# Performance work log

Measured on AMD Instinct MI355X. Metric: run time of the kernel, lower is better.

The kernel has to match this reference:

```python
import jax, jax.numpy as jnp
import numpy as np

B, T, C, HS = 8, 2048, 1024, 64

def setup_inputs() -> dict:
    key = jax.random.key(0)
    kx, kq, kk, kv = jax.random.split(key, 4)
    x = jax.random.normal(kx, (B, T, C), dtype=jnp.float32)
    # Linear(C, HS, bias=False) weights, stored as [C, HS] so projection is x @ W
    Wq = jax.random.normal(kq, (C, HS), dtype=jnp.float32) * (C ** -0.5)
    Wk = jax.random.normal(kk, (C, HS), dtype=jnp.float32) * (C ** -0.5)
    Wv = jax.random.normal(kv, (C, HS), dtype=jnp.float32) * (C ** -0.5)
    return {"x": x, "Wq": Wq, "Wk": Wk, "Wv": Wv}

def reference(x, Wq, Wk, Wv):
    Bq, Tq, Cq = x.shape
    q = x @ Wq  # [B,T,HS]
    k = x @ Wk
    v = x @ Wv
    # NOTE: original scales by C**-0.5 with C = embedding_dim (not head_size)
    att = jnp.einsum('bqd,bkd->bqk', q, k) * (Cq ** -0.5)  # [B,T,T]
    causal = jnp.tril(jnp.ones((Tq, Tq), dtype=bool))
    att = jnp.where(causal, att, -jnp.inf)
    att = jax.nn.softmax(att, axis=-1)
    # dropout p=0.0 -> identity
    y = jnp.einsum('bqk,bkd->bqd', att, v)  # [B,T,HS]
    return y
```

## Files before the change

### kernel.cpp

```cpp
#include <hip/hip_runtime.h>
#include <hip/hip_bf16.h>
#include <math.h>

#define B_   8
#define T_   2048
#define C_   1024
#define HS_  64
#define MTOT (B_*T_)

typedef __attribute__((ext_vector_type(8))) short bf16x8;
typedef __attribute__((ext_vector_type(4))) float f32x4;
typedef __attribute__((ext_vector_type(8))) unsigned short u16x8;

static __device__ __forceinline__ unsigned short f2bf(float f) {
    __hip_bfloat16 h = __float2bfloat16(f);
    return *reinterpret_cast<unsigned short*>(&h);
}

__global__ __launch_bounds__(256) void cast_w_kernel(
    const float* __restrict__ Wq, const float* __restrict__ Wk,
    const float* __restrict__ Wv, unsigned short* __restrict__ Wt)
{
    const int tid = threadIdx.x;
    const int col = tid & 63;
    const int kc  = tid >> 6;
    const int mat = blockIdx.y;
    const int k0  = (blockIdx.x * 4 + kc) * 8;
    const float* __restrict__ W = (mat == 0) ? Wq : (mat == 1) ? Wk : Wv;
    const float s = (mat == 0) ? 0.03125f : 1.0f;

    u16x8 o;
#pragma unroll
    for (int i = 0; i < 8; ++i)
        o[i] = f2bf(W[(size_t)(k0 + i) * HS_ + col] * s);
    *(u16x8*)&Wt[(size_t)(mat * 64 + col) * C_ + k0] = o;
}

__global__ __launch_bounds__(256) void proj_gemm(
    const float* __restrict__ x, const unsigned short* __restrict__ Wt,
    unsigned short* __restrict__ qbf, unsigned short* __restrict__ kbf,
    unsigned short* __restrict__ vtbf)
{
    __shared__ unsigned short Als[2][64][72];
    __shared__ unsigned short Bls[2][64][72];

    const int tid  = threadIdx.x;
    const int lane = tid & 63;
    const int wv   = tid >> 6;
    const int wr   = wv & 1;
    const int wc   = wv >> 1;
    const int g    = lane >> 4;
    const int n15  = lane & 15;
    const int g4   = g * 4;
    const int m0   = blockIdx.x * 64;
    const int mat  = blockIdx.y;

    const int srow = tid >> 2;
    const int kseg = (tid & 3) * 16;
    const float* __restrict__ xrow = &x[(size_t)(m0 + srow) * C_ + kseg];
    const unsigned short* __restrict__ wrow =
        &Wt[(size_t)(mat * 64 + srow) * C_ + kseg];

    f32x4 acc[2][2];
#pragma unroll
    for (int i = 0; i < 2; ++i)
#pragma unroll
        for (int j = 0; j < 2; ++j) acc[i][j] = (f32x4){0.f, 0.f, 0.f, 0.f};

    float4 a0, a1, a2, a3;
    int4   b0, b1;

#define PROJ_LOAD(KC)                                                   \
    do {                                                                \
        a0 = *(const float4*)&xrow[(KC) * 64 + 0];                      \
        a1 = *(const float4*)&xrow[(KC) * 64 + 4];                      \
        a2 = *(const float4*)&xrow[(KC) * 64 + 8];                      \
        a3 = *(const float4*)&xrow[(KC) * 64 + 12];                     \
        b0 = *(const int4*)&wrow[(KC) * 64];                            \
        b1 = *(const int4*)&wrow[(KC) * 64 + 8];                        \
    } while (0)

#define PROJ_WRITE(BUF)                                                 \
    do {                                                                \
        u16x8 v0, v1;                                                   \
        v0[0]=f2bf(a0.x); v0[1]=f2bf(a0.y); v0[2]=f2bf(a0.z); v0[3]=f2bf(a0.w); \
        v0[4]=f2bf(a1.x); v0[5]=f2bf(a1.y); v0[6]=f2bf(a1.z); v0[7]=f2bf(a1.w); \
        v1[0]=f2bf(a2.x); v1[1]=f2bf(a2.y); v1[2]=f2bf(a2.z); v1[3]=f2bf(a2.w); \
        v1[4]=f2bf(a3.x); v1[5]=f2bf(a3.y); v1[6]=f2bf(a3.z); v1[7]=f2bf(a3.w); \
        *(u16x8*)&Als[BUF][srow][kseg]     = v0;                        \
        *(u16x8*)&Als[BUF][srow][kseg + 8] = v1;                        \
        *(int4*)&Bls[BUF][srow][kseg]     = b0;                         \
        *(int4*)&Bls[BUF][srow][kseg + 8] = b1;                         \
    } while (0)

    PROJ_LOAD(0);
    PROJ_WRITE(0);
    __syncthreads();

    for (int kc = 0; kc < C_ / 64; ++kc) {
        const int cur = kc & 1;
        const int kn  = (kc + 1 < C_ / 64) ? kc + 1 : kc;
        PROJ_LOAD(kn);

#pragma unroll
        for (int kk = 0; kk < 2; ++kk) {
            bf16x8 fa0 = *(const bf16x8*)&Als[cur][wr * 32 + n15][kk * 32 + g * 8];
            bf16x8 fa1 = *(const bf16x8*)&Als[cur][wr * 32 + 16 + n15][kk * 32 + g * 8];
            bf16x8 fb0 = *(const bf16x8*)&Bls[cur][wc * 32 + n15][kk * 32 + g * 8];
            bf16x8 fb1 = *(const bf16x8*)&Bls[cur][wc * 32 + 16 + n15][kk * 32 + g * 8];
            acc[0][0] = __builtin_amdgcn_mfma_f32_16x16x32_bf16(fa0, fb0, acc[0][0], 0, 0, 0);
            acc[0][1] = __builtin_amdgcn_mfma_f32_16x16x32_bf16(fa0, fb1, acc[0][1], 0, 0, 0);
            acc[1][0] = __builtin_amdgcn_mfma_f32_16x16x32_bf16(fa1, fb0, acc[1][0], 0, 0, 0);
            acc[1][1] = __builtin_amdgcn_mfma_f32_16x16x32_bf16(fa1, fb1, acc[1][1], 0, 0, 0);
        }

        if (kc + 1 < C_ / 64) {
            __syncthreads();
            PROJ_WRITE(cur ^ 1);
            __syncthreads();
        }
    }
#undef PROJ_LOAD
#undef PROJ_WRITE

    if (mat != 2) {
#pragma unroll
        for (int rf = 0; rf < 2; ++rf)
#pragma unroll
            for (int cf = 0; cf < 2; ++cf) {
                int row = wr * 32 + rf * 16 + g4;
                int col = wc * 32 + cf * 16 + n15;
#pragma unroll
                for (int r = 0; r < 4; ++r)
                    Als[0][row + r][col] = f2bf(acc[rf][cf][r]);
            }
        __syncthreads();
        unsigned short* __restrict__ dst = (mat == 0) ? qbf : kbf;
#pragma unroll
        for (int p = 0; p < 2; ++p) {
            int flat = tid + p * 256;
            int row  = flat >> 3;
            int seg  = (flat & 7) * 8;
            *(int4*)&dst[(size_t)(m0 + row) * HS_ + seg] =
                *(const int4*)&Als[0][row][seg];
        }
    } else {
#pragma unroll
        for (int rf = 0; rf < 2; ++rf)
#pragma unroll
            for (int cf = 0; cf < 2; ++cf) {
                int row = wr * 32 + rf * 16 + g4;
                int col = wc * 32 + cf * 16 + n15;
                ushort4 o;
                o.x = f2bf(acc[rf][cf][0]); o.y = f2bf(acc[rf][cf][1]);
                o.z = f2bf(acc[rf][cf][2]); o.w = f2bf(acc[rf][cf][3]);
                *(ushort4*)&Als[0][col][row] = o;
            }
        __syncthreads();
        const int b  = m0 >> 11;
        const int t0 = m0 & 2047;
        const int hs   = tid >> 2;
        const int tseg = (tid & 3) * 16;
        unsigned short* __restrict__ vdst =
            &vtbf[((size_t)b * HS_ + hs) * T_ + t0 + tseg];
        *(int4*)&vdst[0] = *(const int4*)&Als[0][hs][tseg];
        *(int4*)&vdst[8] = *(const int4*)&Als[0][hs][tseg + 8];
    }
}

__global__ __launch_bounds__(512) void attn_kernel(
    const unsigned short* __restrict__ qbf,
    const unsigned short* __restrict__ kbf,
    const unsigned short* __restrict__ vtbf,
    float* __restrict__ y)
{
    __shared__ unsigned short KVs[4][64][72];

    const int tid  = threadIdx.x;
    const int lane = tid & 63;
    const int wv   = tid >> 6;
    const int rg   = wv & 1;
    const int h    = (wv >> 1) & 1;
    const int tp   = wv >> 2;
    const int g    = lane >> 4;
    const int n15  = lane & 15;
    const int g4   = g * 4;
    const int b    = blockIdx.y;
    const size_t qkoff = (size_t)b * T_ * HS_;
    const size_t voff  = (size_t)b * HS_ * T_;

    const int sgrp = tid >> 8;
    const int st   = tid & 255;
    const int srow = st >> 3;
    const int soff = (st & 7) * 8;

    const unsigned short* __restrict__ kgb = &kbf[qkoff];
    const unsigned short* __restrict__ vgb = &vtbf[voff];

    for (int pass = 0; pass < 2; ++pass) {
        const int qbi  = pass ? (63 - (int)blockIdx.x) : (int)blockIdx.x;
        const int q0   = qbi * 32;
        const int qq0  = q0 + rg * 16;
        const int qrow = qq0 + n15;
        const int nkt  = (qbi >> 1) + 1;

        bf16x8 qf0 = *(const bf16x8*)&qbf[qkoff + (size_t)qrow * HS_ + g * 8];
        bf16x8 qf1 = *(const bf16x8*)&qbf[qkoff + (size_t)qrow * HS_ + g * 8 + 32];

        f32x4 o0 = {0.f,0.f,0.f,0.f}, o1 = o0, o2 = o0, o3 = o0;
        float mrow = -INFINITY, lrow = 0.f;

        int4 kr0, kr1, vr0, vr1;
        {
            int tix = (sgrp < nkt) ? sgrp : nkt - 1;
            kr0 = *(const int4*)&kgb[(size_t)(tix * 64 + srow) * HS_ + soff];
            kr1 = *(const int4*)&kgb[(size_t)(tix * 64 + srow + 32) * HS_ + soff];
            vr0 = *(const int4*)&vgb[(size_t)srow * T_ + tix * 64 + soff];
            vr1 = *(const int4*)&vgb[(size_t)(srow + 32) * T_ + tix * 64 + soff];
        }
        __syncthreads();
        *(int4*)&KVs[sgrp][srow][soff]          = kr0;
        *(int4*)&KVs[sgrp][srow + 32][soff]     = kr1;
        *(int4*)&KVs[2 + sgrp][srow][soff]      = vr0;
        *(int4*)&KVs[2 + sgrp][srow + 32][soff] = vr1;
        __syncthreads();

        const int J = (nkt + 1) >> 1;
        for (int j = 0; j < J; ++j) {
            const int kt = 2 * j + tp;
            {
                int tix = 2 * j + sgrp + 2;
                if (tix > nkt - 1) tix = nkt - 1;
                kr0 = *(const int4*)&kgb[(size_t)(tix * 64 + srow) * HS_ + soff];
                kr1 = *(const int4*)&kgb[(size_t)(tix * 64 + srow + 32) * HS_ + soff];
                vr0 = *(const int4*)&vgb[(size_t)srow * T_ + tix * 64 + soff];
                vr1 = *(const int4*)&vgb[(size_t)(srow + 32) * T_ + tix * 64 + soff];
            }

            if (kt < nkt) {
                const int k0  = kt * 64;
                const int ks0 = h * 32;
                f32x4 st0 = {0.f,0.f,0.f,0.f}, st1 = st0;
                {
                    bf16x8 ka;
                    ka  = *(const bf16x8*)&KVs[tp][ks0 + n15][g * 8];
                    st0 = __builtin_amdgcn_mfma_f32_16x16x32_bf16(ka, qf0, st0, 0, 0, 0);
                    ka  = *(const bf16x8*)&KVs[tp][ks0 + n15][g * 8 + 32];
                    st0 = __builtin_amdgcn_mfma_f32_16x16x32_bf16(ka, qf1, st0, 0, 0, 0);
                    ka  = *(const bf16x8*)&KVs[tp][ks0 + 16 + n15][g * 8];
                    st1 = __builtin_amdgcn_mfma_f32_16x16x32_bf16(ka, qf0, st1, 0, 0, 0);
                    ka  = *(const bf16x8*)&KVs[tp][ks0 + 16 + n15][g * 8 + 32];
                    st1 = __builtin_amdgcn_mfma_f32_16x16x32_bf16(ka, qf1, st1, 0, 0, 0);
                }

                const int kb = k0 + h * 32 + g4;
#pragma unroll
                for (int r = 0; r < 4; ++r) {
                    if (kb + r      > qrow) st0[r] = -INFINITY;
                    if (kb + 16 + r > qrow) st1[r] = -INFINITY;
                }

                float mloc = fmaxf(fmaxf(st0[0], st0[1]), fmaxf(st0[2], st0[3]));
                mloc = fmaxf(mloc, fmaxf(fmaxf(st1[0], st1[1]), fmaxf(st1[2], st1[3])));
                mloc = fmaxf(mloc, __shfl_xor(mloc, 16));
                mloc = fmaxf(mloc, __shfl_xor(mloc, 32));
                float mnew = fmaxf(mrow, mloc);
                float mb   = fmaxf(mnew, -1e30f);
                float corr = __expf(mrow - mb);
                float p[8];
                float psum = 0.f;
#pragma unroll
                for (int r = 0; r < 4; ++r) {
                    p[r]     = __expf(st0[r] - mb);
                    p[4 + r] = __expf(st1[r] - mb);
                    psum += p[r] + p[4 + r];
                }
                psum += __shfl_xor(psum, 16);
                psum += __shfl_xor(psum, 32);
                lrow = lrow * corr + psum;
                mrow = mnew;

#pragma unroll
                for (int r = 0; r < 4; ++r) {
                    float cr = __shfl(corr, g4 + r);
                    o0[r] *= cr; o1[r] *= cr; o2[r] *= cr; o3[r] *= cr;
                }

                bf16x8 pa;
#pragma unroll
                for (int r = 0; r < 4; ++r) {
                    pa[r]     = (short)f2bf(p[r]);
                    pa[4 + r] = (short)f2bf(p[4 + r]);
                }

                const int kvo = h * 32;
                {
                    ushort4 lo, hi; bf16x8 vb;
#define PV_STEP(NT, ONT)                                                        \
                    lo = *(const ushort4*)&KVs[2 + tp][(NT)*16 + n15][kvo + g4];\
                    hi = *(const ushort4*)&KVs[2 + tp][(NT)*16 + n15][kvo + 16 + g4];\
                    vb[0] = (short)lo.x; vb[1] = (short)lo.y;                   \
                    vb[2] = (short)lo.z; vb[3] = (short)lo.w;                   \
                    vb[4] = (short)hi.x; vb[5] = (short)hi.y;                   \
                    vb[6] = (short)hi.z; vb[7] = (short)hi.w;                   \
                    ONT = __builtin_amdgcn_mfma_f32_16x16x32_bf16(pa, vb, ONT, 0, 0, 0);
                    PV_STEP(0, o0)
                    PV_STEP(1, o1)
                    PV_STEP(2, o2)
                    PV_STEP(3, o3)
#undef PV_STEP
                }
            }

            if (j + 1 < J) {
                __syncthreads();
                *(int4*)&KVs[sgrp][srow][soff]          = kr0;
                *(int4*)&KVs[sgrp][srow + 32][soff]     = kr1;
                *(int4*)&KVs[2 + sgrp][srow][soff]      = vr0;
                *(int4*)&KVs[2 + sgrp][srow + 32][soff] = vr1;
                __syncthreads();
            }
        }

        __syncthreads();
        float* FS = (float*)&KVs[0][0][0];
        const int pid = (tp << 1) | h;
        if (pid != 0) {
            float* Ob = FS + (pid - 1) * 2176 + rg * 1088;
#pragma unroll
            for (int r = 0; r < 4; ++r) {
                Ob[(g4 + r) * 68 +  0 + n15] = o0[r];
                Ob[(g4 + r) * 68 + 16 + n15] = o1[r];
                Ob[(g4 + r) * 68 + 32 + n15] = o2[r];
                Ob[(g4 + r) * 68 + 48 + n15] = o3[r];
            }
            if (g == 0) {
                FS[6528 + (pid - 1) * 32 + rg * 16 + n15] = mrow;
                FS[6624 + (pid - 1) * 32 + rg * 16 + n15] = lrow;
            }
        }
        __syncthreads();
        if (pid == 0) {
            float m1 = FS[6528 +  0 + rg * 16 + n15];
            float m2 = FS[6528 + 32 + rg * 16 + n15];
            float m3 = FS[6528 + 64 + rg * 16 + n15];
            float l1 = FS[6624 +  0 + rg * 16 + n15];
            float l2 = FS[6624 + 32 + rg * 16 + n15];
            float l3 = FS[6624 + 64 + rg * 16 + n15];
            float mm = fmaxf(fmaxf(mrow, m1), fmaxf(m2, m3));
            float f0 = __expf(mrow - mm);
            float f1 = __expf(m1 - mm);
            float f2 = __expf(m2 - mm);
            float f3 = __expf(m3 - mm);
            float invl = 1.0f / (lrow * f0 + l1 * f1 + l2 * f2 + l3 * f3);
            const float* O1s = FS;
            const float* O2s = FS + 2176;
            const float* O3s = FS + 4352;
#pragma unroll
            for (int r = 0; r < 4; ++r) {
                float fr0 = __shfl(f0, g4 + r);
                float fr1 = __shfl(f1, g4 + r);
                float fr2 = __shfl(f2, g4 + r);
                float fr3 = __shfl(f3, g4 + r);
                float ir  = __shfl(invl, g4 + r);
                const int base = rg * 1088 + (g4 + r) * 68 + n15;
                float* yr = &y[((size_t)b * T_ + qq0 + g4 + r) * HS_];
                yr[ 0 + n15] = (o0[r] * fr0 + O1s[base]      * fr1 +
                                O2s[base]      * fr2 + O3s[base]      * fr3) * ir;
                yr[16 + n15] = (o1[r] * fr0 + O1s[base + 16] * fr1 +
                                O2s[base + 16] * fr2 + O3s[base + 16] * fr3) * ir;
                yr[32 + n15] = (o2[r] * fr0 + O1s[base + 32] * fr1 +
                                O2s[base + 32] * fr2 + O3s[base + 32] * fr3) * ir;
                yr[48 + n15] = (o3[r] * fr0 + O1s[base + 48] * fr1 +
                                O2s[base + 48] * fr2 + O3s[base + 48] * fr3) * ir;
            }
        }
    }
}

extern "C" void kernel_launch(void* const* d_in, const int* in_sizes, int n_in,
                              void* d_out, int out_size, void* d_ws, size_t ws_size,
                              hipStream_t stream)
{
    const float* x  = (const float*)d_in[0];
    const float* Wq = (const float*)d_in[1];
    const float* Wk = (const float*)d_in[2];
    const float* Wv = (const float*)d_in[3];

    unsigned short* qbf  = (unsigned short*)d_ws;
    unsigned short* kbf  = qbf + (size_t)MTOT * HS_;
    unsigned short* vtbf = kbf + (size_t)MTOT * HS_;
    unsigned short* Wt   = vtbf + (size_t)MTOT * HS_;

    cast_w_kernel<<<dim3(32, 3), 256, 0, stream>>>(Wq, Wk, Wv, Wt);
    proj_gemm<<<dim3(MTOT / 64, 3), 256, 0, stream>>>(x, Wt, qbf, kbf, vtbf);
    attn_kernel<<<dim3(32, B_), 512, 0, stream>>>(qbf, kbf, vtbf, (float*)d_out);
}
```

Baseline: 50.82 us.

## Compute Q, K and V projections in one block to read x once

```diff
diff --git a/kernel.cpp b/kernel.cpp
--- a/kernel.cpp
+++ b/kernel.cpp
@@ -36,61 +36,56 @@
     *(u16x8*)&Wt[(size_t)(mat * 64 + col) * C_ + k0] = o;
 }
 
-__global__ __launch_bounds__(256) void proj_gemm(
+__global__ __launch_bounds__(512) void proj_gemm(
     const float* __restrict__ x, const unsigned short* __restrict__ Wt,
     unsigned short* __restrict__ qbf, unsigned short* __restrict__ kbf,
     unsigned short* __restrict__ vtbf)
 {
     __shared__ unsigned short Als[2][64][72];
-    __shared__ unsigned short Bls[2][64][72];
+    __shared__ unsigned short Bls[2][192][72];
 
     const int tid  = threadIdx.x;
     const int lane = tid & 63;
     const int wv   = tid >> 6;
     const int wr   = wv & 1;
-    const int wc   = wv >> 1;
+    const int cg   = wv >> 1;
     const int g    = lane >> 4;
     const int n15  = lane & 15;
     const int g4   = g * 4;
     const int m0   = blockIdx.x * 64;
-    const int mat  = blockIdx.y;
-
-    const int srow = tid >> 2;
-    const int kseg = (tid & 3) * 16;
-    const float* __restrict__ xrow = &x[(size_t)(m0 + srow) * C_ + kseg];
-    const unsigned short* __restrict__ wrow =
-        &Wt[(size_t)(mat * 64 + srow) * C_ + kseg];
-
-    f32x4 acc[2][2];
+
+    const int srow = tid >> 3;
+    const int seg  = (tid & 7) * 8;
+    const float* __restrict__ xrow = &x[(size_t)(m0 + srow) * C_ + seg];
+    const unsigned short* __restrict__ wrow = &Wt[(size_t)srow * C_ + seg];
+
+    f32x4 acc[2][3];
 #pragma unroll
     for (int i = 0; i < 2; ++i)
 #pragma unroll
-        for (int j = 0; j < 2; ++j) acc[i][j] = (f32x4){0.f, 0.f, 0.f, 0.f};
-
-    float4 a0, a1, a2, a3;
-    int4   b0, b1;
+        for (int j = 0; j < 3; ++j) acc[i][j] = (f32x4){0.f, 0.f, 0.f, 0.f};
+
+    float4 a0, a1;
+    int4   b0, b1, b2;
 
 #define PROJ_LOAD(KC)                                                   \
     do {                                                                \
         a0 = *(const float4*)&xrow[(KC) * 64 + 0];                      \
         a1 = *(const float4*)&xrow[(KC) * 64 + 4];                      \
-        a2 = *(const float4*)&xrow[(KC) * 64 + 8];                      \
-        a3 = *(const float4*)&xrow[(KC) * 64 + 12];                     \
         b0 = *(const int4*)&wrow[(KC) * 64];                            \
-        b1 = *(const int4*)&wrow[(KC) * 64 + 8];                        \
+        b1 = *(const int4*)&wrow[(size_t)64  * C_ + (KC) * 64];        \
+        b2 = *(const int4*)&wrow[(size_t)128 * C_ + (KC) * 64];        \
     } while (0)
 
 #define PROJ_WRITE(BUF)                                                 \
     do {                                                                \
-        u16x8 v0, v1;                                                   \
+        u16x8 v0;                                                       \
         v0[0]=f2bf(a0.x); v0[1]=f2bf(a0.y); v0[2]=f2bf(a0.z); v0[3]=f2bf(a0.w); \
         v0[4]=f2bf(a1.x); v0[5]=f2bf(a1.y); v0[6]=f2bf(a1.z); v0[7]=f2bf(a1.w); \
-        v1[0]=f2bf(a2.x); v1[1]=f2bf(a2.y); v1[2]=f2bf(a2.z); v1[3]=f2bf(a2.w); \
-        v1[4]=f2bf(a3.x); v1[5]=f2bf(a3.y); v1[6]=f2bf(a3.z); v1[7]=f2bf(a3.w); \
-        *(u16x8*)&Als[BUF][srow][kseg]     = v0;                        \
-        *(u16x8*)&Als[BUF][srow][kseg + 8] = v1;                        \
-        *(int4*)&Bls[BUF][srow][kseg]     = b0;                         \
-        *(int4*)&Bls[BUF][srow][kseg + 8] = b1;                         \
+        *(u16x8*)&Als[BUF][srow][seg]       = v0;                       \
+        *(int4*)&Bls[BUF][srow][seg]        = b0;                       \
+        *(int4*)&Bls[BUF][srow + 64][seg]   = b1;                       \
+        *(int4*)&Bls[BUF][srow + 128][seg]  = b2;                       \
     } while (0)
 
     PROJ_LOAD(0);
@@ -106,12 +101,15 @@
         for (int kk = 0; kk < 2; ++kk) {
             bf16x8 fa0 = *(const bf16x8*)&Als[cur][wr * 32 + n15][kk * 32 + g * 8];
             bf16x8 fa1 = *(const bf16x8*)&Als[cur][wr * 32 + 16 + n15][kk * 32 + g * 8];
-            bf16x8 fb0 = *(const bf16x8*)&Bls[cur][wc * 32 + n15][kk * 32 + g * 8];
-            bf16x8 fb1 = *(const bf16x8*)&Bls[cur][wc * 32 + 16 + n15][kk * 32 + g * 8];
+            bf16x8 fb0 = *(const bf16x8*)&Bls[cur][cg * 48 + n15][kk * 32 + g * 8];
+            bf16x8 fb1 = *(const bf16x8*)&Bls[cur][cg * 48 + 16 + n15][kk * 32 + g * 8];
+            bf16x8 fb2 = *(const bf16x8*)&Bls[cur][cg * 48 + 32 + n15][kk * 32 + g * 8];
             acc[0][0] = __builtin_amdgcn_mfma_f32_16x16x32_bf16(fa0, fb0, acc[0][0], 0, 0, 0);
             acc[0][1] = __builtin_amdgcn_mfma_f32_16x16x32_bf16(fa0, fb1, acc[0][1], 0, 0, 0);
+            acc[0][2] = __builtin_amdgcn_mfma_f32_16x16x32_bf16(fa0, fb2, acc[0][2], 0, 0, 0);
             acc[1][0] = __builtin_amdgcn_mfma_f32_16x16x32_bf16(fa1, fb0, acc[1][0], 0, 0, 0);
             acc[1][1] = __builtin_amdgcn_mfma_f32_16x16x32_bf16(fa1, fb1, acc[1][1], 0, 0, 0);
+            acc[1][2] = __builtin_amdgcn_mfma_f32_16x16x32_bf16(fa1, fb2, acc[1][2], 0, 0, 0);
         }
 
         if (kc + 1 < C_ / 64) {
@@ -123,48 +121,45 @@
 #undef PROJ_LOAD
 #undef PROJ_WRITE
 
-    if (mat != 2) {
-#pragma unroll
-        for (int rf = 0; rf < 2; ++rf)
-#pragma unroll
-            for (int cf = 0; cf < 2; ++cf) {
-                int row = wr * 32 + rf * 16 + g4;
-                int col = wc * 32 + cf * 16 + n15;
+    __syncthreads();
+    unsigned short* Cqk = &Als[0][0][0];
+    unsigned short* Vtr = &Bls[0][0][0];
+
+#pragma unroll
+    for (int i = 0; i < 2; ++i)
+#pragma unroll
+        for (int j = 0; j < 3; ++j) {
+            const int gcol = cg * 48 + j * 16 + n15;
+            const int row0 = wr * 32 + i * 16 + g4;
+            if (gcol < 128) {
 #pragma unroll
                 for (int r = 0; r < 4; ++r)
-                    Als[0][row + r][col] = f2bf(acc[rf][cf][r]);
-            }
-        __syncthreads();
-        unsigned short* __restrict__ dst = (mat == 0) ? qbf : kbf;
-#pragma unroll
-        for (int p = 0; p < 2; ++p) {
-            int flat = tid + p * 256;
-            int row  = flat >> 3;
-            int seg  = (flat & 7) * 8;
-            *(int4*)&dst[(size_t)(m0 + row) * HS_ + seg] =
-                *(const int4*)&Als[0][row][seg];
-        }
-    } else {
-#pragma unroll
-        for (int rf = 0; rf < 2; ++rf)
-#pragma unroll
-            for (int cf = 0; cf < 2; ++cf) {
-                int row = wr * 32 + rf * 16 + g4;
-                int col = wc * 32 + cf * 16 + n15;
+                    Cqk[(size_t)(row0 + r) * 136 + gcol] = f2bf(acc[i][j][r]);
+            } else {
                 ushort4 o;
-                o.x = f2bf(acc[rf][cf][0]); o.y = f2bf(acc[rf][cf][1]);
-                o.z = f2bf(acc[rf][cf][2]); o.w = f2bf(acc[rf][cf][3]);
-                *(ushort4*)&Als[0][col][row] = o;
-            }
-        __syncthreads();
+                o.x = f2bf(acc[i][j][0]); o.y = f2bf(acc[i][j][1]);
+                o.z = f2bf(acc[i][j][2]); o.w = f2bf(acc[i][j][3]);
+                *(ushort4*)&Vtr[(size_t)(gcol - 128) * 72 + row0] = o;
+            }
+        }
+    __syncthreads();
+
+#pragma unroll
+    for (int p = 0; p < 2; ++p) {
+        const int flat = tid + p * 512;
+        const int mat  = flat >> 9;
+        const int r64  = (flat >> 3) & 63;
+        const int sg   = (flat & 7) * 8;
+        unsigned short* __restrict__ dst = mat ? kbf : qbf;
+        *(int4*)&dst[(size_t)(m0 + r64) * HS_ + sg] =
+            *(const int4*)&Cqk[(size_t)r64 * 136 + mat * 64 + sg];
+    }
+    {
         const int b  = m0 >> 11;
         const int t0 = m0 & 2047;
-        const int hs   = tid >> 2;
-        const int tseg = (tid & 3) * 16;
-        unsigned short* __restrict__ vdst =
-            &vtbf[((size_t)b * HS_ + hs) * T_ + t0 + tseg];
-        *(int4*)&vdst[0] = *(const int4*)&Als[0][hs][tseg];
-        *(int4*)&vdst[8] = *(const int4*)&Als[0][hs][tseg + 8];
+        const int hs = tid >> 3;
+        *(int4*)&vtbf[((size_t)b * HS_ + hs) * T_ + t0 + seg] =
+            *(const int4*)&Vtr[(size_t)hs * 72 + seg];
     }
 }
 
@@ -393,6 +388,6 @@
     unsigned short* Wt   = vtbf + (size_t)MTOT * HS_;
 
     cast_w_kernel<<<dim3(32, 3), 256, 0, stream>>>(Wq, Wk, Wv, Wt);
-    proj_gemm<<<dim3(MTOT / 64, 3), 256, 0, stream>>>(x, Wt, qbf, kbf, vtbf);
+    proj_gemm<<<256, 512, 0, stream>>>(x, Wt, qbf, kbf, vtbf);
     attn_kernel<<<dim3(32, B_), 512, 0, stream>>>(qbf, kbf, vtbf, (float*)d_out);
 }
```

New measurement: 50.10 us. About the same (-1.4%).
